# Performance work log

Measured on AMD Instinct MI355X. Metric: run time of the kernel, lower is better.

Reference implementation:

```python
import jax, jax.numpy as jnp
import numpy as np

HEADS = 2
NEG_SLOPE = 0.2  # PyG GATConv default leaky_relu slope


def gat_conv(x, edge_index, W, a_src, a_dst, bias, num_nodes):
    """PyG-style GATConv with concat=True and self-loops.
    x: [N, Fin], W: [Fin, H*C], a_src/a_dst: [H, C], bias: [H*C].
    edge_index: [2, E] with row 0 = source j, row 1 = target i.
    """
    H = HEADS
    C = W.shape[1] // H
    # add self loops
    loops = jnp.arange(num_nodes, dtype=edge_index.dtype)
    src = jnp.concatenate([edge_index[0], loops])
    dst = jnp.concatenate([edge_index[1], loops])

    xW = (x @ W).reshape(num_nodes, H, C)            # [N, H, C]
    alpha_s = jnp.einsum('nhc,hc->nh', xW, a_src)    # [N, H]
    alpha_d = jnp.einsum('nhc,hc->nh', xW, a_dst)    # [N, H]
    e = alpha_s[src] + alpha_d[dst]                  # [E, H]
    e = jax.nn.leaky_relu(e, NEG_SLOPE)
    # segment softmax over edges sharing the same target node
    m = jax.ops.segment_max(e, dst, num_segments=num_nodes)  # [N, H]
    e = jnp.exp(e - m[dst])
    denom = jax.ops.segment_sum(e, dst, num_segments=num_nodes)  # [N, H]
    alpha = e / denom[dst]                           # [E, H]
    # message = alpha_ij * xW_j, aggregated at target i
    msg = xW[src] * alpha[:, :, None]                # [E, H, C]
    out = jax.ops.segment_sum(msg, dst, num_segments=num_nodes)  # [N, H, C]
    return out.reshape(num_nodes, H * C) + bias


def setup_inputs() -> dict:
    key = jax.random.key(0)
    ks = jax.random.split(key, 10)
    N, E = 50000, 800000
    Fin, D = 128, 128
    H = HEADS
    x = jax.random.normal(ks[0], (N, Fin), dtype=jnp.float32)
    edge_index = jax.random.randint(ks[1], (2, E), 0, N, dtype=jnp.int64)
    g = 1.0 / np.sqrt(Fin)
    W1 = jax.random.normal(ks[2], (Fin, H * D), dtype=jnp.float32) * g
    a_src1 = jax.random.normal(ks[3], (H, D), dtype=jnp.float32) * g
    a_dst1 = jax.random.normal(ks[4], (H, D), dtype=jnp.float32) * g
    b1 = jnp.zeros((H * D,), dtype=jnp.float32)
    g2 = 1.0 / np.sqrt(H * D)
    W2 = jax.random.normal(ks[5], (H * D, H * D), dtype=jnp.float32) * g2
    a_src2 = jax.random.normal(ks[6], (H, D), dtype=jnp.float32) * g2
    a_dst2 = jax.random.normal(ks[7], (H, D), dtype=jnp.float32) * g2
    b2 = jnp.zeros((H * D,), dtype=jnp.float32)
    return {"x": x, "edge_index": edge_index,
            "W1": W1, "a_src1": a_src1, "a_dst1": a_dst1, "b1": b1,
            "W2": W2, "a_src2": a_src2, "a_dst2": a_dst2, "b2": b2}


def reference(x, edge_index, W1, a_src1, a_dst1, b1, W2, a_src2, a_dst2, b2):
    N = x.shape[0]
    h = gat_conv(x, edge_index, W1, a_src1, a_dst1, b1, N)
    h = jax.nn.elu(h)
    # dropout is identity in eval mode (deterministic reference)
    out = gat_conv(h, edge_index, W2, a_src2, a_dst2, b2, N)
    return out
```

## Files before the change

### kernel.cpp

```cpp
#include <hip/hip_runtime.h>
#include <math.h>

#define HEADS 2
#define CH    128
#define HC    256
#define NEG   0.2f

typedef __attribute__((ext_vector_type(8))) short  bfrag8;
typedef __attribute__((ext_vector_type(4))) float  f32x4;

__device__ inline unsigned short f2bf_rne(float x) {
    unsigned u = __float_as_uint(x);
    u += 0x7fffu + ((u >> 16) & 1u);
    return (unsigned short)(u >> 16);
}
__device__ inline void split2(float x, unsigned short& hi, unsigned short& lo) {
    unsigned u = __float_as_uint(x);
    unsigned r = u + 0x7fffu + ((u >> 16) & 1u);
    unsigned short h = (unsigned short)(r >> 16);
    float hf = __uint_as_float((unsigned)h << 16);
    hi = h;
    lo = f2bf_rne(x - hf);
}

__global__ __launch_bounds__(256)
void wsplit_kernel(const float* __restrict__ W, unsigned short* __restrict__ Whi,
                   unsigned short* __restrict__ Wlo, int K) {
    const int idx = blockIdx.x * 256 + threadIdx.x;
    if (idx >= K * HC) return;
    const int k = idx >> 8;
    const int n = idx & 255;
    unsigned short h, l;
    split2(W[idx], h, l);
    Whi[(size_t)n * K + k] = h;
    Wlo[(size_t)n * K + k] = l;
}

__global__ __launch_bounds__(256)
void gemm_fused_kernel(const float* __restrict__ A,
                       const unsigned short* __restrict__ Wthi,
                       const unsigned short* __restrict__ Wtlo,
                       const float* __restrict__ a_src,
                       const float* __restrict__ a_dst,
                       unsigned short* __restrict__ xWb,
                       float* __restrict__ as_out, float* __restrict__ ad_out,
                       int M, int K) {
    __shared__ unsigned short Ah[128][40];
    __shared__ unsigned short Al[128][40];
    __shared__ unsigned short Bh[128][40];
    __shared__ unsigned short Bl[128][40];

    const int t    = threadIdx.x;
    const int row0 = blockIdx.x * 128;
    const int col0 = blockIdx.y * 128;
    const int lane = t & 63;
    const int wid  = t >> 6;
    const int wr   = wid >> 1;
    const int wc   = wid & 1;

    f32x4 acc[4][4] = {};

    const int ar  = t >> 3;
    const int ac4 = (t & 7) * 4;
    const int bcol   = t >> 1;
    const int bplane = t & 1;

    for (int kk = 0; kk < K; kk += 32) {
        #pragma unroll
        for (int rep = 0; rep < 4; ++rep) {
            const int row = ar + rep * 32;
            const int gr  = row0 + row;
            float4 v = make_float4(0.f, 0.f, 0.f, 0.f);
            if (gr < M)
                v = *reinterpret_cast<const float4*>(&A[(size_t)gr * K + kk + ac4]);
            ushort4 hv, lv;
            split2(v.x, hv.x, lv.x);
            split2(v.y, hv.y, lv.y);
            split2(v.z, hv.z, lv.z);
            split2(v.w, hv.w, lv.w);
            *reinterpret_cast<ushort4*>(&Ah[row][ac4]) = hv;
            *reinterpret_cast<ushort4*>(&Al[row][ac4]) = lv;
        }
        {
            const unsigned short* srcp =
                (bplane ? Wtlo : Wthi) + (size_t)(col0 + bcol) * K + kk;
            unsigned short (*dst)[40] = bplane ? Bl : Bh;
            #pragma unroll
            for (int q = 0; q < 4; ++q) {
                bfrag8 v = *reinterpret_cast<const bfrag8*>(srcp + q * 8);
                *reinterpret_cast<bfrag8*>(&dst[bcol][q * 8]) = v;
            }
        }
        __syncthreads();

        bfrag8 ah[4], al[4], bh[4], bl[4];
        const int ko = (lane >> 4) * 8;
        #pragma unroll
        for (int m = 0; m < 4; ++m) {
            const int row = wr * 64 + m * 16 + (lane & 15);
            ah[m] = *reinterpret_cast<const bfrag8*>(&Ah[row][ko]);
            al[m] = *reinterpret_cast<const bfrag8*>(&Al[row][ko]);
        }
        #pragma unroll
        for (int n = 0; n < 4; ++n) {
            const int col = wc * 64 + n * 16 + (lane & 15);
            bh[n] = *reinterpret_cast<const bfrag8*>(&Bh[col][ko]);
            bl[n] = *reinterpret_cast<const bfrag8*>(&Bl[col][ko]);
        }

        #pragma unroll
        for (int m = 0; m < 4; ++m)
            #pragma unroll
            for (int n = 0; n < 4; ++n) {
                acc[m][n] = __builtin_amdgcn_mfma_f32_16x16x32_bf16(al[m], bh[n], acc[m][n], 0, 0, 0);
                acc[m][n] = __builtin_amdgcn_mfma_f32_16x16x32_bf16(ah[m], bl[n], acc[m][n], 0, 0, 0);
                acc[m][n] = __builtin_amdgcn_mfma_f32_16x16x32_bf16(ah[m], bh[n], acc[m][n], 0, 0, 0);
            }
        __syncthreads();
    }

    __shared__ float s_lds[2][128];
    __shared__ float d_lds[2][128];

    float asv[4], adv[4];
    #pragma unroll
    for (int n = 0; n < 4; ++n) {
        const int gc = col0 + wc * 64 + n * 16 + (lane & 15);
        asv[n] = a_src[gc];
        adv[n] = a_dst[gc];
    }

    #pragma unroll
    for (int m = 0; m < 4; ++m) {
        #pragma unroll
        for (int reg = 0; reg < 4; ++reg) {
            const int row = wr * 64 + m * 16 + (lane >> 4) * 4 + reg;
            const int gr  = row0 + row;
            float ps = acc[m][0][reg] * asv[0] + acc[m][1][reg] * asv[1] +
                       acc[m][2][reg] * asv[2] + acc[m][3][reg] * asv[3];
            float pd = acc[m][0][reg] * adv[0] + acc[m][1][reg] * adv[1] +
                       acc[m][2][reg] * adv[2] + acc[m][3][reg] * adv[3];
            #pragma unroll
            for (int msk = 1; msk <= 8; msk <<= 1) {
                ps += __shfl_xor(ps, msk);
                pd += __shfl_xor(pd, msk);
            }
            if ((lane & 15) == 0) {
                s_lds[wc][row] = ps;
                d_lds[wc][row] = pd;
            }
            if (gr < M) {
                unsigned short* rp = &xWb[(size_t)gr * HC + col0];
                #pragma unroll
                for (int n = 0; n < 4; ++n)
                    rp[wc * 64 + n * 16 + (lane & 15)] = f2bf_rne(acc[m][n][reg]);
            }
        }
    }
    __syncthreads();
    if (t < 128) {
        const int gr = row0 + t;
        if (gr < M) {
            as_out[gr * 2 + blockIdx.y] = s_lds[0][t] + s_lds[1][t];
            ad_out[gr * 2 + blockIdx.y] = d_lds[0][t] + d_lds[1][t];
        }
    }
}

__global__ __launch_bounds__(256)
void hist_kernel(const int* __restrict__ dst, int* __restrict__ counts, int E) {
    const int e = blockIdx.x * 256 + threadIdx.x;
    if (e < E) atomicAdd(&counts[dst[e]], 1);
}

__global__ __launch_bounds__(256)
void scan_local_kernel(int* __restrict__ data, int* __restrict__ chunk_sum, int N) {
    __shared__ int s[256];
    const int t   = threadIdx.x;
    const int idx = blockIdx.x * 256 + t;
    const int v   = (idx < N) ? data[idx] : 0;
    s[t] = v;
    __syncthreads();
    #pragma unroll
    for (int off = 1; off < 256; off <<= 1) {
        int x = (t >= off) ? s[t - off] : 0;
        __syncthreads();
        s[t] += x;
        __syncthreads();
    }
    if (idx < N) data[idx] = s[t] - v;
    if (t == 255) chunk_sum[blockIdx.x] = s[255];
}

__global__ __launch_bounds__(256)
void scan_chunks_kernel(int* __restrict__ chunk, int nb) {
    __shared__ int s[256];
    const int t = threadIdx.x;
    const int v = (t < nb) ? chunk[t] : 0;
    s[t] = v;
    __syncthreads();
    #pragma unroll
    for (int off = 1; off < 256; off <<= 1) {
        int x = (t >= off) ? s[t - off] : 0;
        __syncthreads();
        s[t] += x;
        __syncthreads();
    }
    if (t < nb) chunk[t] = s[t] - v;
}

__global__ __launch_bounds__(256)
void add_offsets_kernel(const int* __restrict__ excl, const int* __restrict__ chunk_excl,
                        int* __restrict__ row_ptr, int* __restrict__ cursor,
                        int N, int E) {
    const int idx = blockIdx.x * 256 + threadIdx.x;
    if (idx < N) {
        const int rp = excl[idx] + chunk_excl[idx >> 8];
        row_ptr[idx] = rp;
        cursor[idx]  = rp;
    }
    if (idx == 0) row_ptr[N] = E;
}

__global__ __launch_bounds__(256)
void scatter_kernel(const int* __restrict__ src, const int* __restrict__ dst,
                    int* __restrict__ cursor, int* __restrict__ col_idx, int E) {
    const int e = blockIdx.x * 256 + threadIdx.x;
    if (e < E) {
        const int pos = atomicAdd(&cursor[dst[e]], 1);
        col_idx[pos] = src[e];
    }
}

__global__ __launch_bounds__(256)
void agg_kernel(const int* __restrict__ row_ptr, const int* __restrict__ col_idx,
                const unsigned short* __restrict__ xWb,
                const float* __restrict__ as_, const float* __restrict__ ad_,
                const float* __restrict__ bias, float* __restrict__ out,
                int N, int do_elu) {
    const int wv   = (blockIdx.x * 256 + threadIdx.x) >> 6;
    const int lane = threadIdx.x & 63;
    if (wv >= N) return;
    const int i    = wv;
    const int half = lane >> 5;
    const int sl   = lane & 31;
    const int hh   = sl >> 4;
    const int cb   = hh * 128 + (sl & 15) * 8;
    const float adi = ad_[i * 2 + hh];

    float acc[8] = {};
    float dn = 0.f;

    const int beg = row_ptr[i];
    const int end = row_ptr[i + 1];

    int k = beg + half;
    int j = (k < end) ? col_idx[k] : 0;
    for (; k < end; k += 2) {
        const int jn = (k + 2 < end) ? col_idx[k + 2] : 0;
        float e = as_[j * 2 + hh] + adi;
        e = e > 0.f ? e : NEG * e;
        const float w = expf(e);
        const uint4 q = *reinterpret_cast<const uint4*>(&xWb[(size_t)j * HC + cb]);
        const unsigned qq[4] = {q.x, q.y, q.z, q.w};
        #pragma unroll
        for (int r = 0; r < 4; ++r) {
            const float flo = __uint_as_float(qq[r] << 16);
            const float fhi = __uint_as_float(qq[r] & 0xffff0000u);
            acc[r * 2 + 0] = fmaf(w, flo, acc[r * 2 + 0]);
            acc[r * 2 + 1] = fmaf(w, fhi, acc[r * 2 + 1]);
        }
        dn += w;
        j = jn;
    }

    #pragma unroll
    for (int r = 0; r < 8; ++r) acc[r] += __shfl_xor(acc[r], 32);
    dn += __shfl_xor(dn, 32);

    if (lane < 32) {
        float e = as_[i * 2 + hh] + adi;
        e = e > 0.f ? e : NEG * e;
        const float ws = expf(e);
        const uint4 q = *reinterpret_cast<const uint4*>(&xWb[(size_t)i * HC + cb]);
        const unsigned qq[4] = {q.x, q.y, q.z, q.w};
        #pragma unroll
        for (int r = 0; r < 4; ++r) {
            const float flo = __uint_as_float(qq[r] << 16);
            const float fhi = __uint_as_float(qq[r] & 0xffff0000u);
            acc[r * 2 + 0] = fmaf(ws, flo, acc[r * 2 + 0]);
            acc[r * 2 + 1] = fmaf(ws, fhi, acc[r * 2 + 1]);
        }
        dn += ws;

        const float inv = 1.f / dn;
        const float4 b0 = *reinterpret_cast<const float4*>(&bias[cb]);
        const float4 b1 = *reinterpret_cast<const float4*>(&bias[cb + 4]);
        float o[8];
        o[0] = acc[0] * inv + b0.x; o[1] = acc[1] * inv + b0.y;
        o[2] = acc[2] * inv + b0.z; o[3] = acc[3] * inv + b0.w;
        o[4] = acc[4] * inv + b1.x; o[5] = acc[5] * inv + b1.y;
        o[6] = acc[6] * inv + b1.z; o[7] = acc[7] * inv + b1.w;
        if (do_elu) {
            #pragma unroll
            for (int r = 0; r < 8; ++r) o[r] = o[r] > 0.f ? o[r] : expm1f(o[r]);
        }
        *reinterpret_cast<float4*>(&out[(size_t)i * HC + cb]) =
            make_float4(o[0], o[1], o[2], o[3]);
        *reinterpret_cast<float4*>(&out[(size_t)i * HC + cb + 4]) =
            make_float4(o[4], o[5], o[6], o[7]);
    }
}

extern "C" void kernel_launch(void* const* d_in, const int* in_sizes, int n_in,
                              void* d_out, int out_size, void* d_ws, size_t ws_size,
                              hipStream_t stream) {
    const float* x      = (const float*)d_in[0];
    const int*   ei     = (const int*)d_in[1];
    const float* W1     = (const float*)d_in[2];
    const float* a_src1 = (const float*)d_in[3];
    const float* a_dst1 = (const float*)d_in[4];
    const float* b1     = (const float*)d_in[5];
    const float* W2     = (const float*)d_in[6];
    const float* a_src2 = (const float*)d_in[7];
    const float* a_dst2 = (const float*)d_in[8];
    const float* b2     = (const float*)d_in[9];
    float* out = (float*)d_out;

    const int Nn = in_sizes[0] / 128;
    const int E  = in_sizes[1] / 2;
    const int K1 = in_sizes[2] / HC;
    const int* src = ei;
    const int* dst = ei + E;

    float* bufB  = (float*)d_ws;
    float* as_b  = bufB + (size_t)Nn * HC;
    float* ad_b  = as_b + (size_t)Nn * 2;
    int*   tmp   = (int*)(ad_b + (size_t)Nn * 2);
    int*   chunk = tmp + Nn;
    int*   rowp  = chunk + 256;
    int*   curs  = rowp + (Nn + 1);
    int*   colx  = curs + Nn;
    unsigned short* wt1hi = (unsigned short*)(colx + E);
    unsigned short* wt1lo = wt1hi + (size_t)HC * K1;
    unsigned short* wt2hi = wt1lo + (size_t)HC * K1;
    unsigned short* wt2lo = wt2hi + (size_t)HC * HC;
    unsigned short* xWb   = wt2lo + (size_t)HC * HC;

    const int nb = (Nn + 255) / 256;

    wsplit_kernel<<<(K1 * HC + 255) / 256, 256, 0, stream>>>(W1, wt1hi, wt1lo, K1);
    wsplit_kernel<<<(HC * HC + 255) / 256, 256, 0, stream>>>(W2, wt2hi, wt2lo, HC);

    hipMemsetAsync(tmp, 0, (size_t)Nn * sizeof(int), stream);
    hist_kernel<<<(E + 255) / 256, 256, 0, stream>>>(dst, tmp, E);
    scan_local_kernel<<<nb, 256, 0, stream>>>(tmp, chunk, Nn);
    scan_chunks_kernel<<<1, 256, 0, stream>>>(chunk, nb);
    add_offsets_kernel<<<nb, 256, 0, stream>>>(tmp, chunk, rowp, curs, Nn, E);
    scatter_kernel<<<(E + 255) / 256, 256, 0, stream>>>(src, dst, curs, colx, E);

    const dim3 ggrid((Nn + 127) / 128, HC / 128);
    const int  agrid = (Nn + 3) / 4;

    gemm_fused_kernel<<<ggrid, 256, 0, stream>>>(x, wt1hi, wt1lo, a_src1, a_dst1,
                                                 xWb, as_b, ad_b, Nn, K1);
    agg_kernel<<<agrid, 256, 0, stream>>>(rowp, colx, xWb, as_b, ad_b, b1, bufB, Nn, 1);

    gemm_fused_kernel<<<ggrid, 256, 0, stream>>>(bufB, wt2hi, wt2lo, a_src2, a_dst2,
                                                 xWb, as_b, ad_b, Nn, HC);
    agg_kernel<<<agrid, 256, 0, stream>>>(rowp, colx, xWb, as_b, ad_b, b2, out, Nn, 0);
}
```

Baseline: 352.2 us.

## Pre-split GEMM inputs to bf16 hi/lo and widen aggregation to four edge streams

Adds a kernel that splits x into bf16 hi/lo planes up front, and makes layer-1 aggregation write its ELU output directly as bf16 hi/lo planes. The GEMM then loads pre-split operands instead of converting fp32 tiles inside the block. This moves the split arithmetic out of both column blocks of each GEMM, so it runs once per element rather than once per block. The aggregation kernel now processes four neighbour edges in parallel per wave, with 16 channels per lane, and prefetches the next attention score. The cost is an extra pass over x, more workspace, and a wider shuffle reduction.

```diff
diff --git a/kernel.cpp b/kernel.cpp
--- a/kernel.cpp
+++ b/kernel.cpp
@@ -37,7 +37,23 @@
 }
 
 __global__ __launch_bounds__(256)
-void gemm_fused_kernel(const float* __restrict__ A,
+void asplit_kernel(const float* __restrict__ A, unsigned short* __restrict__ Ahi,
+                   unsigned short* __restrict__ Alo, int total4) {
+    const int idx = blockIdx.x * 256 + threadIdx.x;
+    if (idx >= total4) return;
+    const float4 v = *reinterpret_cast<const float4*>(&A[idx * 4]);
+    ushort4 hv, lv;
+    split2(v.x, hv.x, lv.x);
+    split2(v.y, hv.y, lv.y);
+    split2(v.z, hv.z, lv.z);
+    split2(v.w, hv.w, lv.w);
+    *reinterpret_cast<ushort4*>(&Ahi[idx * 4]) = hv;
+    *reinterpret_cast<ushort4*>(&Alo[idx * 4]) = lv;
+}
+
+__global__ __launch_bounds__(256)
+void gemm_fused_kernel(const unsigned short* __restrict__ Ahi,
+                       const unsigned short* __restrict__ Alo,
                        const unsigned short* __restrict__ Wthi,
                        const unsigned short* __restrict__ Wtlo,
                        const float* __restrict__ a_src,
@@ -60,26 +76,24 @@
 
     f32x4 acc[4][4] = {};
 
-    const int ar  = t >> 3;
-    const int ac4 = (t & 7) * 4;
+    const int ar  = t >> 2;
+    const int ac8 = (t & 3) * 8;
     const int bcol   = t >> 1;
     const int bplane = t & 1;
 
     for (int kk = 0; kk < K; kk += 32) {
         #pragma unroll
-        for (int rep = 0; rep < 4; ++rep) {
-            const int row = ar + rep * 32;
+        for (int rep = 0; rep < 2; ++rep) {
+            const int row = ar + rep * 64;
             const int gr  = row0 + row;
-            float4 v = make_float4(0.f, 0.f, 0.f, 0.f);
-            if (gr < M)
-                v = *reinterpret_cast<const float4*>(&A[(size_t)gr * K + kk + ac4]);
-            ushort4 hv, lv;
-            split2(v.x, hv.x, lv.x);
-            split2(v.y, hv.y, lv.y);
-            split2(v.z, hv.z, lv.z);
-            split2(v.w, hv.w, lv.w);
-            *reinterpret_cast<ushort4*>(&Ah[row][ac4]) = hv;
-            *reinterpret_cast<ushort4*>(&Al[row][ac4]) = lv;
+            bfrag8 vh = {0, 0, 0, 0, 0, 0, 0, 0};
+            bfrag8 vl = {0, 0, 0, 0, 0, 0, 0, 0};
+            if (gr < M) {
+                vh = *reinterpret_cast<const bfrag8*>(&Ahi[(size_t)gr * K + kk + ac8]);
+                vl = *reinterpret_cast<const bfrag8*>(&Alo[(size_t)gr * K + kk + ac8]);
+            }
+            *reinterpret_cast<bfrag8*>(&Ah[row][ac8]) = vh;
+            *reinterpret_cast<bfrag8*>(&Al[row][ac8]) = vl;
         }
         {
             const unsigned short* srcp =
@@ -236,56 +250,66 @@
 void agg_kernel(const int* __restrict__ row_ptr, const int* __restrict__ col_idx,
                 const unsigned short* __restrict__ xWb,
                 const float* __restrict__ as_, const float* __restrict__ ad_,
-                const float* __restrict__ bias, float* __restrict__ out,
-                int N, int do_elu) {
+                const float* __restrict__ bias, float* __restrict__ outf,
+                unsigned short* __restrict__ outhi, unsigned short* __restrict__ outlo,
+                int N, int mode) {
     const int wv   = (blockIdx.x * 256 + threadIdx.x) >> 6;
     const int lane = threadIdx.x & 63;
     if (wv >= N) return;
-    const int i    = wv;
-    const int half = lane >> 5;
-    const int sl   = lane & 31;
-    const int hh   = sl >> 4;
-    const int cb   = hh * 128 + (sl & 15) * 8;
-    const float adi = ad_[i * 2 + hh];
-
-    float acc[8] = {};
+    const int i      = wv;
+    const int stream = lane >> 4;
+    const int sl     = lane & 15;
+    const int hh     = sl >> 3;
+    const int cb     = sl * 16;
+    const float adi  = ad_[i * 2 + hh];
+
+    float acc[16] = {};
     float dn = 0.f;
 
     const int beg = row_ptr[i];
     const int end = row_ptr[i + 1];
 
-    int k = beg + half;
+    int k = beg + stream;
     int j = (k < end) ? col_idx[k] : 0;
-    for (; k < end; k += 2) {
-        const int jn = (k + 2 < end) ? col_idx[k + 2] : 0;
-        float e = as_[j * 2 + hh] + adi;
+    float asj = as_[j * 2 + hh];
+    for (; k < end; k += 4) {
+        const int kn = k + 4;
+        const int jn = (kn < end) ? col_idx[kn] : 0;
+        const float asn = as_[jn * 2 + hh];
+        float e = asj + adi;
         e = e > 0.f ? e : NEG * e;
         const float w = expf(e);
-        const uint4 q = *reinterpret_cast<const uint4*>(&xWb[(size_t)j * HC + cb]);
-        const unsigned qq[4] = {q.x, q.y, q.z, q.w};
-        #pragma unroll
-        for (int r = 0; r < 4; ++r) {
+        const uint4 q0 = *reinterpret_cast<const uint4*>(&xWb[(size_t)j * HC + cb]);
+        const uint4 q1 = *reinterpret_cast<const uint4*>(&xWb[(size_t)j * HC + cb + 8]);
+        const unsigned qq[8] = {q0.x, q0.y, q0.z, q0.w, q1.x, q1.y, q1.z, q1.w};
+        #pragma unroll
+        for (int r = 0; r < 8; ++r) {
             const float flo = __uint_as_float(qq[r] << 16);
             const float fhi = __uint_as_float(qq[r] & 0xffff0000u);
             acc[r * 2 + 0] = fmaf(w, flo, acc[r * 2 + 0]);
             acc[r * 2 + 1] = fmaf(w, fhi, acc[r * 2 + 1]);
         }
         dn += w;
-        j = jn;
+        j = jn; asj = asn;
     }
 
     #pragma unroll
-    for (int r = 0; r < 8; ++r) acc[r] += __shfl_xor(acc[r], 32);
+    for (int r = 0; r < 16; ++r) {
+        acc[r] += __shfl_xor(acc[r], 16);
+        acc[r] += __shfl_xor(acc[r], 32);
+    }
+    dn += __shfl_xor(dn, 16);
     dn += __shfl_xor(dn, 32);
 
-    if (lane < 32) {
+    if (lane < 16) {
         float e = as_[i * 2 + hh] + adi;
         e = e > 0.f ? e : NEG * e;
         const float ws = expf(e);
-        const uint4 q = *reinterpret_cast<const uint4*>(&xWb[(size_t)i * HC + cb]);
-        const unsigned qq[4] = {q.x, q.y, q.z, q.w};
-        #pragma unroll
-        for (int r = 0; r < 4; ++r) {
+        const uint4 q0 = *reinterpret_cast<const uint4*>(&xWb[(size_t)i * HC + cb]);
+        const uint4 q1 = *reinterpret_cast<const uint4*>(&xWb[(size_t)i * HC + cb + 8]);
+        const unsigned qq[8] = {q0.x, q0.y, q0.z, q0.w, q1.x, q1.y, q1.z, q1.w};
+        #pragma unroll
+        for (int r = 0; r < 8; ++r) {
             const float flo = __uint_as_float(qq[r] << 16);
             const float fhi = __uint_as_float(qq[r] & 0xffff0000u);
             acc[r * 2 + 0] = fmaf(ws, flo, acc[r * 2 + 0]);
@@ -294,21 +318,34 @@
         dn += ws;
 
         const float inv = 1.f / dn;
-        const float4 b0 = *reinterpret_cast<const float4*>(&bias[cb]);
-        const float4 b1 = *reinterpret_cast<const float4*>(&bias[cb + 4]);
-        float o[8];
-        o[0] = acc[0] * inv + b0.x; o[1] = acc[1] * inv + b0.y;
-        o[2] = acc[2] * inv + b0.z; o[3] = acc[3] * inv + b0.w;
-        o[4] = acc[4] * inv + b1.x; o[5] = acc[5] * inv + b1.y;
-        o[6] = acc[6] * inv + b1.z; o[7] = acc[7] * inv + b1.w;
-        if (do_elu) {
-            #pragma unroll
-            for (int r = 0; r < 8; ++r) o[r] = o[r] > 0.f ? o[r] : expm1f(o[r]);
-        }
-        *reinterpret_cast<float4*>(&out[(size_t)i * HC + cb]) =
-            make_float4(o[0], o[1], o[2], o[3]);
-        *reinterpret_cast<float4*>(&out[(size_t)i * HC + cb + 4]) =
-            make_float4(o[4], o[5], o[6], o[7]);
+        float o[16];
+        #pragma unroll
+        for (int r = 0; r < 4; ++r) {
+            const float4 b4 = *reinterpret_cast<const float4*>(&bias[cb + r * 4]);
+            o[r * 4 + 0] = acc[r * 4 + 0] * inv + b4.x;
+            o[r * 4 + 1] = acc[r * 4 + 1] * inv + b4.y;
+            o[r * 4 + 2] = acc[r * 4 + 2] * inv + b4.z;
+            o[r * 4 + 3] = acc[r * 4 + 3] * inv + b4.w;
+        }
+        if (mode) {
+            #pragma unroll
+            for (int r = 0; r < 16; ++r) o[r] = o[r] > 0.f ? o[r] : expm1f(o[r]);
+            #pragma unroll
+            for (int r = 0; r < 4; ++r) {
+                ushort4 hv, lv;
+                split2(o[r * 4 + 0], hv.x, lv.x);
+                split2(o[r * 4 + 1], hv.y, lv.y);
+                split2(o[r * 4 + 2], hv.z, lv.z);
+                split2(o[r * 4 + 3], hv.w, lv.w);
+                *reinterpret_cast<ushort4*>(&outhi[(size_t)i * HC + cb + r * 4]) = hv;
+                *reinterpret_cast<ushort4*>(&outlo[(size_t)i * HC + cb + r * 4]) = lv;
+            }
+        } else {
+            #pragma unroll
+            for (int r = 0; r < 4; ++r)
+                *reinterpret_cast<float4*>(&outf[(size_t)i * HC + cb + r * 4]) =
+                    make_float4(o[r * 4 + 0], o[r * 4 + 1], o[r * 4 + 2], o[r * 4 + 3]);
+        }
     }
 }
 
@@ -333,8 +370,7 @@
     const int* src = ei;
     const int* dst = ei + E;
 
-    float* bufB  = (float*)d_ws;
-    float* as_b  = bufB + (size_t)Nn * HC;
+    float* as_b  = (float*)d_ws;
     float* ad_b  = as_b + (size_t)Nn * 2;
     int*   tmp   = (int*)(ad_b + (size_t)Nn * 2);
     int*   chunk = tmp + Nn;
@@ -346,11 +382,16 @@
     unsigned short* wt2hi = wt1lo + (size_t)HC * K1;
     unsigned short* wt2lo = wt2hi + (size_t)HC * HC;
     unsigned short* xWb   = wt2lo + (size_t)HC * HC;
+    unsigned short* xhi   = xWb + (size_t)Nn * HC;
+    unsigned short* xlo   = xhi + (size_t)Nn * K1;
+    unsigned short* hhi   = xlo + (size_t)Nn * K1;
+    unsigned short* hlo   = hhi + (size_t)Nn * HC;
 
     const int nb = (Nn + 255) / 256;
 
     wsplit_kernel<<<(K1 * HC + 255) / 256, 256, 0, stream>>>(W1, wt1hi, wt1lo, K1);
     wsplit_kernel<<<(HC * HC + 255) / 256, 256, 0, stream>>>(W2, wt2hi, wt2lo, HC);
+    asplit_kernel<<<(Nn * K1 / 4 + 255) / 256, 256, 0, stream>>>(x, xhi, xlo, Nn * K1 / 4);
 
     hipMemsetAsync(tmp, 0, (size_t)Nn * sizeof(int), stream);
     hist_kernel<<<(E + 255) / 256, 256, 0, stream>>>(dst, tmp, E);
@@ -362,11 +403,14 @@
     const dim3 ggrid((Nn + 127) / 128, HC / 128);
     const int  agrid = (Nn + 3) / 4;
 
-    gemm_fused_kernel<<<ggrid, 256, 0, stream>>>(x, wt1hi, wt1lo, a_src1, a_dst1,
+    gemm_fused_kernel<<<ggrid, 256, 0, stream>>>(xhi, xlo, wt1hi, wt1lo, a_src1, a_dst1,
                                                  xWb, as_b, ad_b, Nn, K1);
-    agg_kernel<<<agrid, 256, 0, stream>>>(rowp, colx, xWb, as_b, ad_b, b1, bufB, Nn, 1);
-
-    gemm_fused_kernel<<<ggrid, 256, 0, stream>>>(bufB, wt2hi, wt2lo, a_src2, a_dst2,
+    agg_kernel<<<agrid, 256, 0, stream>>>(rowp, colx, xWb, as_b, ad_b, b1,
+                                          (float*)nullptr, hhi, hlo, Nn, 1);
+
+    gemm_fused_kernel<<<ggrid, 256, 0, stream>>>(hhi, hlo, wt2hi, wt2lo, a_src2, a_dst2,
                                                  xWb, as_b, ad_b, Nn, HC);
-    agg_kernel<<<agrid, 256, 0, stream>>>(rowp, colx, xWb, as_b, ad_b, b2, out, Nn, 0);
-}
+    agg_kernel<<<agrid, 256, 0, stream>>>(rowp, colx, xWb, as_b, ad_b, b2,
+                                          out, (unsigned short*)nullptr,
+                                          (unsigned short*)nullptr, Nn, 0);
+}
```

After: 365.9 us. 1.04x slower.

## Drop split-bf16 GEMM, precompute W·a vectors for attention logits

Applied to the files above, without the earlier changes.

Replaces the three-MFMA hi/lo split-bf16 GEMM with a single plain bf16 GEMM on pre-cast bf16 inputs. The attention logits are now computed as x·(W·a) using fp32 vectors precomputed per layer. For layer 1 these logits come from a separate x-prep pass, and for layer 2 they are fused into the layer-1 aggregation epilogue, which also writes h directly as bf16. This cuts GEMM MFMA work, removes fp32 A-operand conversion from the GEMM, and halves the intermediate h traffic. In exchange, the message features lose precision because the low-order bf16 correction term is gone.

```diff
diff --git a/kernel.cpp b/kernel.cpp
--- a/kernel.cpp
+++ b/kernel.cpp
@@ -14,41 +14,73 @@
     u += 0x7fffu + ((u >> 16) & 1u);
     return (unsigned short)(u >> 16);
 }
-__device__ inline void split2(float x, unsigned short& hi, unsigned short& lo) {
-    unsigned u = __float_as_uint(x);
-    unsigned r = u + 0x7fffu + ((u >> 16) & 1u);
-    unsigned short h = (unsigned short)(r >> 16);
-    float hf = __uint_as_float((unsigned)h << 16);
-    hi = h;
-    lo = f2bf_rne(x - hf);
-}
-
-__global__ __launch_bounds__(256)
-void wsplit_kernel(const float* __restrict__ W, unsigned short* __restrict__ Whi,
-                   unsigned short* __restrict__ Wlo, int K) {
+
+__global__ __launch_bounds__(256)
+void wcast_kernel(const float* __restrict__ W, unsigned short* __restrict__ Wt, int K) {
     const int idx = blockIdx.x * 256 + threadIdx.x;
     if (idx >= K * HC) return;
     const int k = idx >> 8;
     const int n = idx & 255;
-    unsigned short h, l;
-    split2(W[idx], h, l);
-    Whi[(size_t)n * K + k] = h;
-    Wlo[(size_t)n * K + k] = l;
-}
-
-__global__ __launch_bounds__(256)
-void gemm_fused_kernel(const float* __restrict__ A,
-                       const unsigned short* __restrict__ Wthi,
-                       const unsigned short* __restrict__ Wtlo,
-                       const float* __restrict__ a_src,
-                       const float* __restrict__ a_dst,
-                       unsigned short* __restrict__ xWb,
-                       float* __restrict__ as_out, float* __restrict__ ad_out,
-                       int M, int K) {
+    Wt[(size_t)n * K + k] = f2bf_rne(W[idx]);
+}
+
+__global__ __launch_bounds__(256)
+void va_kernel(const float* __restrict__ W, const float* __restrict__ a_src,
+               const float* __restrict__ a_dst, float* __restrict__ va, int K) {
+    const int k    = (blockIdx.x * 256 + threadIdx.x) >> 6;
+    const int lane = threadIdx.x & 63;
+    if (k >= K) return;
+    const int c0 = lane * 4;
+    const float4 w4 = *reinterpret_cast<const float4*>(&W[(size_t)k * HC + c0]);
+    const float4 s4 = *reinterpret_cast<const float4*>(&a_src[c0]);
+    const float4 d4 = *reinterpret_cast<const float4*>(&a_dst[c0]);
+    float ps = w4.x * s4.x + w4.y * s4.y + w4.z * s4.z + w4.w * s4.w;
+    float pd = w4.x * d4.x + w4.y * d4.y + w4.z * d4.z + w4.w * d4.w;
+    #pragma unroll
+    for (int m = 1; m <= 16; m <<= 1) {
+        ps += __shfl_xor(ps, m);
+        pd += __shfl_xor(pd, m);
+    }
+    if (lane == 0)  { va[k * 4 + 0] = ps; va[k * 4 + 2] = pd; }
+    if (lane == 32) { va[k * 4 + 1] = ps; va[k * 4 + 3] = pd; }
+}
+
+__global__ __launch_bounds__(256)
+void xprep_kernel(const float* __restrict__ x, const float* __restrict__ va,
+                  unsigned short* __restrict__ xb, float* __restrict__ as_out,
+                  float* __restrict__ ad_out, int N, int K) {
+    const int i    = (blockIdx.x * 256 + threadIdx.x) >> 6;
+    const int lane = threadIdx.x & 63;
+    if (i >= N) return;
+    const float2 v = reinterpret_cast<const float2*>(&x[(size_t)i * K])[lane];
+    ushort2 bv; bv.x = f2bf_rne(v.x); bv.y = f2bf_rne(v.y);
+    reinterpret_cast<ushort2*>(&xb[(size_t)i * K])[lane] = bv;
+
+    const float4 a0 = reinterpret_cast<const float4*>(va)[lane * 2 + 0];
+    const float4 a1 = reinterpret_cast<const float4*>(va)[lane * 2 + 1];
+    float p0 = v.x * a0.x + v.y * a1.x;
+    float p1 = v.x * a0.y + v.y * a1.y;
+    float p2 = v.x * a0.z + v.y * a1.z;
+    float p3 = v.x * a0.w + v.y * a1.w;
+    #pragma unroll
+    for (int m = 1; m <= 32; m <<= 1) {
+        p0 += __shfl_xor(p0, m);
+        p1 += __shfl_xor(p1, m);
+        p2 += __shfl_xor(p2, m);
+        p3 += __shfl_xor(p3, m);
+    }
+    if (lane == 0) {
+        as_out[i * 2 + 0] = p0; as_out[i * 2 + 1] = p1;
+        ad_out[i * 2 + 0] = p2; ad_out[i * 2 + 1] = p3;
+    }
+}
+
+__global__ __launch_bounds__(256)
+void gemm_msg_kernel(const unsigned short* __restrict__ Ab,
+                     const unsigned short* __restrict__ Wt,
+                     unsigned short* __restrict__ xWb, int M, int K) {
     __shared__ unsigned short Ah[128][40];
-    __shared__ unsigned short Al[128][40];
     __shared__ unsigned short Bh[128][40];
-    __shared__ unsigned short Bl[128][40];
 
     const int t    = threadIdx.x;
     const int row0 = blockIdx.x * 128;
@@ -60,109 +92,56 @@
 
     f32x4 acc[4][4] = {};
 
-    const int ar  = t >> 3;
-    const int ac4 = (t & 7) * 4;
-    const int bcol   = t >> 1;
-    const int bplane = t & 1;
+    const int arow = t & 127;
+    const int aseg = (t >> 7) * 16;
 
     for (int kk = 0; kk < K; kk += 32) {
-        #pragma unroll
-        for (int rep = 0; rep < 4; ++rep) {
-            const int row = ar + rep * 32;
-            const int gr  = row0 + row;
-            float4 v = make_float4(0.f, 0.f, 0.f, 0.f);
-            if (gr < M)
-                v = *reinterpret_cast<const float4*>(&A[(size_t)gr * K + kk + ac4]);
-            ushort4 hv, lv;
-            split2(v.x, hv.x, lv.x);
-            split2(v.y, hv.y, lv.y);
-            split2(v.z, hv.z, lv.z);
-            split2(v.w, hv.w, lv.w);
-            *reinterpret_cast<ushort4*>(&Ah[row][ac4]) = hv;
-            *reinterpret_cast<ushort4*>(&Al[row][ac4]) = lv;
-        }
         {
-            const unsigned short* srcp =
-                (bplane ? Wtlo : Wthi) + (size_t)(col0 + bcol) * K + kk;
-            unsigned short (*dst)[40] = bplane ? Bl : Bh;
-            #pragma unroll
-            for (int q = 0; q < 4; ++q) {
-                bfrag8 v = *reinterpret_cast<const bfrag8*>(srcp + q * 8);
-                *reinterpret_cast<bfrag8*>(&dst[bcol][q * 8]) = v;
-            }
-        }
-        __syncthreads();
-
-        bfrag8 ah[4], al[4], bh[4], bl[4];
+            const int gr = row0 + arow;
+            bfrag8 v0 = {0,0,0,0,0,0,0,0}, v1 = {0,0,0,0,0,0,0,0};
+            if (gr < M) {
+                v0 = *reinterpret_cast<const bfrag8*>(&Ab[(size_t)gr * K + kk + aseg]);
+                v1 = *reinterpret_cast<const bfrag8*>(&Ab[(size_t)gr * K + kk + aseg + 8]);
+            }
+            *reinterpret_cast<bfrag8*>(&Ah[arow][aseg])     = v0;
+            *reinterpret_cast<bfrag8*>(&Ah[arow][aseg + 8]) = v1;
+            const bfrag8 w0 = *reinterpret_cast<const bfrag8*>(
+                &Wt[(size_t)(col0 + arow) * K + kk + aseg]);
+            const bfrag8 w1 = *reinterpret_cast<const bfrag8*>(
+                &Wt[(size_t)(col0 + arow) * K + kk + aseg + 8]);
+            *reinterpret_cast<bfrag8*>(&Bh[arow][aseg])     = w0;
+            *reinterpret_cast<bfrag8*>(&Bh[arow][aseg + 8]) = w1;
+        }
+        __syncthreads();
+
+        bfrag8 ah[4], bh[4];
         const int ko = (lane >> 4) * 8;
         #pragma unroll
-        for (int m = 0; m < 4; ++m) {
-            const int row = wr * 64 + m * 16 + (lane & 15);
-            ah[m] = *reinterpret_cast<const bfrag8*>(&Ah[row][ko]);
-            al[m] = *reinterpret_cast<const bfrag8*>(&Al[row][ko]);
-        }
-        #pragma unroll
-        for (int n = 0; n < 4; ++n) {
-            const int col = wc * 64 + n * 16 + (lane & 15);
-            bh[n] = *reinterpret_cast<const bfrag8*>(&Bh[col][ko]);
-            bl[n] = *reinterpret_cast<const bfrag8*>(&Bl[col][ko]);
-        }
-
-        #pragma unroll
         for (int m = 0; m < 4; ++m)
-            #pragma unroll
-            for (int n = 0; n < 4; ++n) {
-                acc[m][n] = __builtin_amdgcn_mfma_f32_16x16x32_bf16(al[m], bh[n], acc[m][n], 0, 0, 0);
-                acc[m][n] = __builtin_amdgcn_mfma_f32_16x16x32_bf16(ah[m], bl[n], acc[m][n], 0, 0, 0);
+            ah[m] = *reinterpret_cast<const bfrag8*>(&Ah[wr * 64 + m * 16 + (lane & 15)][ko]);
+        #pragma unroll
+        for (int n = 0; n < 4; ++n)
+            bh[n] = *reinterpret_cast<const bfrag8*>(&Bh[wc * 64 + n * 16 + (lane & 15)][ko]);
+
+        #pragma unroll
+        for (int m = 0; m < 4; ++m)
+            #pragma unroll
+            for (int n = 0; n < 4; ++n)
                 acc[m][n] = __builtin_amdgcn_mfma_f32_16x16x32_bf16(ah[m], bh[n], acc[m][n], 0, 0, 0);
-            }
-        __syncthreads();
-    }
-
-    __shared__ float s_lds[2][128];
-    __shared__ float d_lds[2][128];
-
-    float asv[4], adv[4];
-    #pragma unroll
-    for (int n = 0; n < 4; ++n) {
-        const int gc = col0 + wc * 64 + n * 16 + (lane & 15);
-        asv[n] = a_src[gc];
-        adv[n] = a_dst[gc];
+        __syncthreads();
     }
 
     #pragma unroll
     for (int m = 0; m < 4; ++m) {
         #pragma unroll
         for (int reg = 0; reg < 4; ++reg) {
-            const int row = wr * 64 + m * 16 + (lane >> 4) * 4 + reg;
-            const int gr  = row0 + row;
-            float ps = acc[m][0][reg] * asv[0] + acc[m][1][reg] * asv[1] +
-                       acc[m][2][reg] * asv[2] + acc[m][3][reg] * asv[3];
-            float pd = acc[m][0][reg] * adv[0] + acc[m][1][reg] * adv[1] +
-                       acc[m][2][reg] * adv[2] + acc[m][3][reg] * adv[3];
-            #pragma unroll
-            for (int msk = 1; msk <= 8; msk <<= 1) {
-                ps += __shfl_xor(ps, msk);
-                pd += __shfl_xor(pd, msk);
-            }
-            if ((lane & 15) == 0) {
-                s_lds[wc][row] = ps;
-                d_lds[wc][row] = pd;
-            }
+            const int gr = row0 + wr * 64 + m * 16 + (lane >> 4) * 4 + reg;
             if (gr < M) {
                 unsigned short* rp = &xWb[(size_t)gr * HC + col0];
                 #pragma unroll
                 for (int n = 0; n < 4; ++n)
                     rp[wc * 64 + n * 16 + (lane & 15)] = f2bf_rne(acc[m][n][reg]);
             }
-        }
-    }
-    __syncthreads();
-    if (t < 128) {
-        const int gr = row0 + t;
-        if (gr < M) {
-            as_out[gr * 2 + blockIdx.y] = s_lds[0][t] + s_lds[1][t];
-            ad_out[gr * 2 + blockIdx.y] = d_lds[0][t] + d_lds[1][t];
         }
     }
 }
@@ -236,8 +215,10 @@
 void agg_kernel(const int* __restrict__ row_ptr, const int* __restrict__ col_idx,
                 const unsigned short* __restrict__ xWb,
                 const float* __restrict__ as_, const float* __restrict__ ad_,
-                const float* __restrict__ bias, float* __restrict__ out,
-                int N, int do_elu) {
+                const float* __restrict__ bias, float* __restrict__ outf,
+                unsigned short* __restrict__ hb, const float* __restrict__ va,
+                float* __restrict__ as2, float* __restrict__ ad2,
+                int N, int mode) {
     const int wv   = (blockIdx.x * 256 + threadIdx.x) >> 6;
     const int lane = threadIdx.x & 63;
     if (wv >= N) return;
@@ -256,9 +237,12 @@
 
     int k = beg + half;
     int j = (k < end) ? col_idx[k] : 0;
+    float asj = as_[j * 2 + hh];
     for (; k < end; k += 2) {
-        const int jn = (k + 2 < end) ? col_idx[k + 2] : 0;
-        float e = as_[j * 2 + hh] + adi;
+        const int kn = k + 2;
+        const int jn = (kn < end) ? col_idx[kn] : 0;
+        const float asn = as_[jn * 2 + hh];
+        float e = asj + adi;
         e = e > 0.f ? e : NEG * e;
         const float w = expf(e);
         const uint4 q = *reinterpret_cast<const uint4*>(&xWb[(size_t)j * HC + cb]);
@@ -271,7 +255,7 @@
             acc[r * 2 + 1] = fmaf(w, fhi, acc[r * 2 + 1]);
         }
         dn += w;
-        j = jn;
+        j = jn; asj = asn;
     }
 
     #pragma unroll
@@ -301,14 +285,40 @@
         o[2] = acc[2] * inv + b0.z; o[3] = acc[3] * inv + b0.w;
         o[4] = acc[4] * inv + b1.x; o[5] = acc[5] * inv + b1.y;
         o[6] = acc[6] * inv + b1.z; o[7] = acc[7] * inv + b1.w;
-        if (do_elu) {
+
+        if (mode) {
             #pragma unroll
             for (int r = 0; r < 8; ++r) o[r] = o[r] > 0.f ? o[r] : expm1f(o[r]);
-        }
-        *reinterpret_cast<float4*>(&out[(size_t)i * HC + cb]) =
-            make_float4(o[0], o[1], o[2], o[3]);
-        *reinterpret_cast<float4*>(&out[(size_t)i * HC + cb + 4]) =
-            make_float4(o[4], o[5], o[6], o[7]);
+            bfrag8 hv;
+            #pragma unroll
+            for (int r = 0; r < 8; ++r) hv[r] = (short)f2bf_rne(o[r]);
+            *reinterpret_cast<bfrag8*>(&hb[(size_t)i * HC + cb]) = hv;
+            float p0 = 0.f, p1 = 0.f, p2 = 0.f, p3 = 0.f;
+            #pragma unroll
+            for (int r = 0; r < 8; ++r) {
+                const float4 vv = reinterpret_cast<const float4*>(va)[cb + r];
+                p0 = fmaf(o[r], vv.x, p0);
+                p1 = fmaf(o[r], vv.y, p1);
+                p2 = fmaf(o[r], vv.z, p2);
+                p3 = fmaf(o[r], vv.w, p3);
+            }
+            #pragma unroll
+            for (int m = 1; m <= 16; m <<= 1) {
+                p0 += __shfl_xor(p0, m);
+                p1 += __shfl_xor(p1, m);
+                p2 += __shfl_xor(p2, m);
+                p3 += __shfl_xor(p3, m);
+            }
+            if (sl == 0) {
+                as2[i * 2 + 0] = p0; as2[i * 2 + 1] = p1;
+                ad2[i * 2 + 0] = p2; ad2[i * 2 + 1] = p3;
+            }
+        } else {
+            *reinterpret_cast<float4*>(&outf[(size_t)i * HC + cb]) =
+                make_float4(o[0], o[1], o[2], o[3]);
+            *reinterpret_cast<float4*>(&outf[(size_t)i * HC + cb + 4]) =
+                make_float4(o[4], o[5], o[6], o[7]);
+        }
     }
 }
 
@@ -333,24 +343,31 @@
     const int* src = ei;
     const int* dst = ei + E;
 
-    float* bufB  = (float*)d_ws;
-    float* as_b  = bufB + (size_t)Nn * HC;
-    float* ad_b  = as_b + (size_t)Nn * 2;
-    int*   tmp   = (int*)(ad_b + (size_t)Nn * 2);
+    float* as1   = (float*)d_ws;
+    float* ad1   = as1 + (size_t)Nn * 2;
+    float* as2   = ad1 + (size_t)Nn * 2;
+    float* ad2   = as2 + (size_t)Nn * 2;
+    float* va1   = ad2 + (size_t)Nn * 2;
+    float* va2   = va1 + (size_t)K1 * 4;
+    int*   tmp   = (int*)(va2 + (size_t)HC * 4);
     int*   chunk = tmp + Nn;
     int*   rowp  = chunk + 256;
     int*   curs  = rowp + (Nn + 1);
     int*   colx  = curs + Nn;
-    unsigned short* wt1hi = (unsigned short*)(colx + E);
-    unsigned short* wt1lo = wt1hi + (size_t)HC * K1;
-    unsigned short* wt2hi = wt1lo + (size_t)HC * K1;
-    unsigned short* wt2lo = wt2hi + (size_t)HC * HC;
-    unsigned short* xWb   = wt2lo + (size_t)HC * HC;
+    uintptr_t pa = ((uintptr_t)(colx + E) + 31) & ~(uintptr_t)31;
+    unsigned short* wt1 = (unsigned short*)pa;
+    unsigned short* wt2 = wt1 + (size_t)HC * K1;
+    unsigned short* xb  = wt2 + (size_t)HC * HC;
+    unsigned short* xWb = xb  + (size_t)Nn * K1;
+    unsigned short* hb  = xWb + (size_t)Nn * HC;
 
     const int nb = (Nn + 255) / 256;
 
-    wsplit_kernel<<<(K1 * HC + 255) / 256, 256, 0, stream>>>(W1, wt1hi, wt1lo, K1);
-    wsplit_kernel<<<(HC * HC + 255) / 256, 256, 0, stream>>>(W2, wt2hi, wt2lo, HC);
+    wcast_kernel<<<(K1 * HC + 255) / 256, 256, 0, stream>>>(W1, wt1, K1);
+    wcast_kernel<<<(HC * HC + 255) / 256, 256, 0, stream>>>(W2, wt2, HC);
+    va_kernel<<<(K1 + 3) / 4, 256, 0, stream>>>(W1, a_src1, a_dst1, va1, K1);
+    va_kernel<<<(HC + 3) / 4, 256, 0, stream>>>(W2, a_src2, a_dst2, va2, HC);
+    xprep_kernel<<<(Nn + 3) / 4, 256, 0, stream>>>(x, va1, xb, as1, ad1, Nn, K1);
 
     hipMemsetAsync(tmp, 0, (size_t)Nn * sizeof(int), stream);
     hist_kernel<<<(E + 255) / 256, 256, 0, stream>>>(dst, tmp, E);
@@ -362,11 +379,13 @@
     const dim3 ggrid((Nn + 127) / 128, HC / 128);
     const int  agrid = (Nn + 3) / 4;
 
-    gemm_fused_kernel<<<ggrid, 256, 0, stream>>>(x, wt1hi, wt1lo, a_src1, a_dst1,
-                                                 xWb, as_b, ad_b, Nn, K1);
-    agg_kernel<<<agrid, 256, 0, stream>>>(rowp, colx, xWb, as_b, ad_b, b1, bufB, Nn, 1);
-
-    gemm_fused_kernel<<<ggrid, 256, 0, stream>>>(bufB, wt2hi, wt2lo, a_src2, a_dst2,
-                                                 xWb, as_b, ad_b, Nn, HC);
-    agg_kernel<<<agrid, 256, 0, stream>>>(rowp, colx, xWb, as_b, ad_b, b2, out, Nn, 0);
-}
+    gemm_msg_kernel<<<ggrid, 256, 0, stream>>>(xb, wt1, xWb, Nn, K1);
+    agg_kernel<<<agrid, 256, 0, stream>>>(rowp, colx, xWb, as1, ad1, b1,
+                                          (float*)nullptr, hb, va2, as2, ad2, Nn, 1);
+
+    gemm_msg_kernel<<<ggrid, 256, 0, stream>>>(hb, wt2, xWb, Nn, HC);
+    agg_kernel<<<agrid, 256, 0, stream>>>(rowp, colx, xWb, as2, ad2, b2,
+                                          out, (unsigned short*)nullptr,
+                                          (const float*)nullptr,
+                                          (float*)nullptr, (float*)nullptr, Nn, 0);
+}
```

Measured after the change: 335.5 us. -4.7%, faster.
